# Performance work log

Measured on AMD Instinct MI355X. Metric: run time of the kernel, lower is better.

## Reference

```python
import jax, jax.numpy as jnp
import numpy as np

NUM_EXPERTS = 8
TOP_K = 2

def setup_inputs() -> dict:
    key = jax.random.key(0)
    k1, k2, k3, k4 = jax.random.split(key, 4)
    B, T, C, F = 4, 2048, 1024, 4096
    x = jax.random.normal(k1, (B, T, C), dtype=jnp.float32)
    gate_w = jax.random.normal(k2, (C, NUM_EXPERTS), dtype=jnp.float32) * 0.02
    w1 = jax.random.normal(k3, (NUM_EXPERTS, C, F), dtype=jnp.float32) * 0.02
    w2 = jax.random.normal(k4, (NUM_EXPERTS, F, C), dtype=jnp.float32) * 0.02
    return {"x": x, "gate_w": gate_w, "w1": w1, "w2": w2}

def reference(x, gate_w, w1, w2):
    # Router: softmax over experts, then top-k and renormalize
    router_logits = jnp.einsum('btc,ce->bte', x, gate_w)          # [B,T,E]
    routing = jax.nn.softmax(router_logits, axis=-1)
    topw, topi = jax.lax.top_k(routing, TOP_K)                    # [B,T,K]
    topw = topw / jnp.sum(topw, axis=-1, keepdims=True)
    # Combined per-expert weight per token (zero if not selected)
    onehot = jax.nn.one_hot(topi, NUM_EXPERTS, dtype=x.dtype)     # [B,T,K,E]
    combine = jnp.einsum('btk,btke->bte', topw, onehot)           # [B,T,E]
    # Expert FFNs (exact GELU, matching torch nn.GELU default)
    out = jnp.zeros_like(x)
    for e in range(NUM_EXPERTS):
        h = jax.nn.gelu(jnp.einsum('btc,cf->btf', x, w1[e]), approximate=False)
        y = jnp.einsum('btf,fc->btc', h, w2[e])
        out = out + combine[..., e:e+1] * y
    return out
```

## Files before the change

kernel.cpp:

```cpp
#include <hip/hip_runtime.h>
#include <hip/hip_bf16.h>
#include <math.h>

#define NUM_EXPERTS 8
#define NTOK 8192
#define CDIM 1024
#define FDIM 4096
#define MAXSLOTS 17408
#define MAXTILES 136
#define TILES_PER_XCD 17

typedef __bf16 bf16x8 __attribute__((ext_vector_type(8)));
typedef float  f32x4  __attribute__((ext_vector_type(4)));

#define GPTR(p) ((const __attribute__((address_space(1))) unsigned int*)(p))
#define LPTR(p) ((__attribute__((address_space(3))) unsigned int*)(p))

__device__ __forceinline__ float gelu_exact(float v){
  return 0.5f * v * (1.0f + erff(v * 0.70710678118654752f));
}
__device__ __forceinline__ float bf2f(unsigned short u){
  union { unsigned int i; float f; } cv; cv.i = ((unsigned int)u) << 16; return cv.f;
}

__global__ __launch_bounds__(256) void moe_router(
    const float* __restrict__ x, const float* __restrict__ gw,
    int2* __restrict__ topi, float2* __restrict__ topw, int* __restrict__ counts)
{
  int token = blockIdx.x * 4 + (threadIdx.x >> 6);
  int lane  = threadIdx.x & 63;
  int e = lane & 7, part = lane >> 3;
  const float* xr = x + (size_t)token * CDIM;
  float s = 0.f;
  int c0 = part * 128;
  for (int c = c0; c < c0 + 128; ++c) s += xr[c] * gw[c * 8 + e];
  s += __shfl_xor(s, 8); s += __shfl_xor(s, 16); s += __shfl_xor(s, 32);
  float m1 = s; int i1 = e;
  for (int off = 1; off < 8; off <<= 1){
    float ov = __shfl_xor(m1, off); int oi = __shfl_xor(i1, off);
    if (ov > m1 || (ov == m1 && oi < i1)){ m1 = ov; i1 = oi; }
  }
  float l2 = (e == i1) ? -INFINITY : s;
  float m2 = l2; int i2 = e;
  for (int off = 1; off < 8; off <<= 1){
    float ov = __shfl_xor(m2, off); int oi = __shfl_xor(i2, off);
    if (ov > m2 || (ov == m2 && oi < i2)){ m2 = ov; i2 = oi; }
  }
  if (lane == 0){
    float r = expf(m2 - m1);
    float wa = 1.f / (1.f + r);
    topi[token] = make_int2(i1, i2);
    topw[token] = make_float2(wa, 1.f - wa);
    atomicAdd(&counts[i1], 1);
    atomicAdd(&counts[i2], 1);
  }
}

__global__ __launch_bounds__(256) void convert_x_kernel(
    const float* __restrict__ x, __hip_bfloat16* __restrict__ xb)
{
  int i = (blockIdx.x * 256 + threadIdx.x) * 4;
  float4 v = *(const float4*)(x + i);
  union { __hip_bfloat16 hh[4]; ushort4 u; } cv;
  cv.hh[0] = __float2bfloat16(v.x);
  cv.hh[1] = __float2bfloat16(v.y);
  cv.hh[2] = __float2bfloat16(v.z);
  cv.hh[3] = __float2bfloat16(v.w);
  *(ushort4*)(xb + i) = cv.u;
}

__global__ __launch_bounds__(256) void transpose_bf16_kernel(
    const float* __restrict__ in, __hip_bfloat16* __restrict__ outp, int R, int Cc)
{
  __shared__ __hip_bfloat16 tile[64 * 66];
  const size_t msz = (size_t)R * Cc;
  const float* inm = in + (size_t)blockIdx.z * msz;
  __hip_bfloat16* outm = outp + (size_t)blockIdx.z * msz;
  int r0 = blockIdx.y * 64, c0 = blockIdx.x * 64;
  int t = threadIdx.x;
  int r = t & 63, cseg = (t >> 6) * 16;
  const float* src = inm + (size_t)(r0 + r) * Cc + c0 + cseg;
  float4 v0 = ((const float4*)src)[0];
  float4 v1 = ((const float4*)src)[1];
  float4 v2 = ((const float4*)src)[2];
  float4 v3 = ((const float4*)src)[3];
  float vv[16] = {v0.x,v0.y,v0.z,v0.w, v1.x,v1.y,v1.z,v1.w,
                  v2.x,v2.y,v2.z,v2.w, v3.x,v3.y,v3.z,v3.w};
#pragma unroll
  for (int k = 0; k < 16; ++k)
    tile[(cseg + k) * 66 + r] = __float2bfloat16(vv[k]);
  __syncthreads();
#pragma unroll
  for (int p = 0; p < 2; ++p){
    int cc = p * 32 + (t >> 3), ch = (t & 7) * 8;
    const unsigned short* rowp = (const unsigned short*)tile + cc * 66 + ch;
    unsigned int a = *(const unsigned int*)(rowp + 0);
    unsigned int b = *(const unsigned int*)(rowp + 2);
    unsigned int c = *(const unsigned int*)(rowp + 4);
    unsigned int d = *(const unsigned int*)(rowp + 6);
    *(uint4*)(outm + (size_t)(c0 + cc) * R + r0 + ch) = make_uint4(a, b, c, d);
  }
}

__global__ void scan_kernel(const int* __restrict__ counts, int* cursors, int* num_tiles,
    int* tile_expert, int* tile_slotbase, int* slot_token, float* slot_weight)
{
  int t = threadIdx.x;
  if (t == 0){
    int base = 0, T = 0;
    for (int e = 0; e < NUM_EXPERTS; ++e){
      cursors[e] = base;
      int nt = (counts[e] + 127) >> 7;
      for (int i = 0; i < nt; ++i){ tile_expert[T] = e; tile_slotbase[T] = base + i * 128; ++T; }
      base += nt << 7;
    }
    *num_tiles = T;
  }
  for (int i = t; i < MAXSLOTS; i += 256){ slot_token[i] = 0; slot_weight[i] = 0.f; }
}

__global__ void assign_kernel(const int2* __restrict__ topi, const float2* __restrict__ topw,
    int* cursors, int* slot_token, float* slot_weight, int2* __restrict__ token_slots)
{
  int token = blockIdx.x * 256 + threadIdx.x;
  int2 ii = topi[token];
  float2 ww = topw[token];
  int p0 = atomicAdd(&cursors[ii.x], 1);
  slot_token[p0] = token; slot_weight[p0] = ww.x;
  int p1 = atomicAdd(&cursors[ii.y], 1);
  slot_token[p1] = token; slot_weight[p1] = ww.y;
  token_slots[token] = make_int2(p0, p1);
}

__global__ __launch_bounds__(256) void gemm1_kernel(
    const __hip_bfloat16* __restrict__ xbf, const __hip_bfloat16* __restrict__ w1t,
    __hip_bfloat16* __restrict__ h, const int* __restrict__ num_tiles,
    const int* __restrict__ tile_expert, const int* __restrict__ tile_slotbase,
    const int* __restrict__ slot_token)
{
  __shared__ __align__(16) char smem[32768];
  const int L = blockIdx.x;
  const int xcd = L & 7;
  const int j = L >> 3;
  const int tl = j >> 5;
  const int nb = j & 31;
  const int tm = xcd * TILES_PER_XCD + tl;
  if (tm >= *num_tiles) return;
  const int e = tile_expert[tm];
  const int sbase = tile_slotbase[tm];
  const int n0 = nb * 128;
  const int t = threadIdx.x;
  const int cl = t & 7;
  const __hip_bfloat16* w1e = w1t + (size_t)e * FDIM * CDIM;
  const __hip_bfloat16* aptr[4];
  const __hip_bfloat16* bptr[4];
#pragma unroll
  for (int jj = 0; jj < 4; ++jj){
    int r = jj * 32 + (t >> 3);
    int cg = cl ^ (r & 7);
    int tok = slot_token[sbase + r];
    aptr[jj] = xbf + (size_t)tok * CDIM + cg * 8;
    bptr[jj] = w1e + (size_t)(n0 + r) * CDIM + cg * 8;
  }
  char* asml = smem + t * 16;
  char* bsml = smem + 16384 + t * 16;

  f32x4 acc[4][4] = {};
  const int lane = t & 63, wv = t >> 6;
  const int wm = (wv >> 1) * 64, wn = (wv & 1) * 64;
  const int lrow = lane & 15, quad = lane >> 4;

  for (int k0 = 0; k0 < CDIM; k0 += 64){
    __syncthreads();
#pragma unroll
    for (int jj = 0; jj < 4; ++jj){
      __builtin_amdgcn_global_load_lds(GPTR(aptr[jj] + k0), LPTR(asml + jj * 4096), 16, 0, 0);
      __builtin_amdgcn_global_load_lds(GPTR(bptr[jj] + k0), LPTR(bsml + jj * 4096), 16, 0, 0);
    }
    __syncthreads();
#pragma unroll
    for (int kk = 0; kk < 2; ++kk){
      bf16x8 af[4], bfr[4];
#pragma unroll
      for (int i = 0; i < 4; ++i){
        int ar = wm + i * 16 + lrow;
        int ac = (kk * 4 + quad) ^ (ar & 7);
        af[i] = *(const bf16x8*)(smem + ar * 128 + ac * 16);
        int br = wn + i * 16 + lrow;
        int bc = (kk * 4 + quad) ^ (br & 7);
        bfr[i] = *(const bf16x8*)(smem + 16384 + br * 128 + bc * 16);
      }
#pragma unroll
      for (int i = 0; i < 4; ++i)
#pragma unroll
        for (int jj = 0; jj < 4; ++jj)
          acc[i][jj] = __builtin_amdgcn_mfma_f32_16x16x32_bf16(af[i], bfr[jj], acc[i][jj], 0, 0, 0);
    }
  }
  __syncthreads();
  __hip_bfloat16* Ct = (__hip_bfloat16*)smem;
#pragma unroll
  for (int i = 0; i < 4; ++i)
#pragma unroll
    for (int r = 0; r < 4; ++r){
      int row = wm + i * 16 + quad * 4 + r;
#pragma unroll
      for (int jj = 0; jj < 4; ++jj){
        int col = wn + jj * 16 + lrow;
        int cc = (col >> 3) ^ (row & 15);
        Ct[row * 128 + cc * 8 + (col & 7)] = __float2bfloat16(gelu_exact(acc[i][jj][r]));
      }
    }
  __syncthreads();
#pragma unroll
  for (int v = 0; v < 8; ++v){
    int Lr = v * 256 + t;
    int row = Lr >> 4, cc = Lr & 15;
    int cs = cc ^ (row & 15);
    uint4 val = *(const uint4*)(Ct + row * 128 + cs * 8);
    *(uint4*)(h + (size_t)(sbase + row) * FDIM + n0 + cc * 8) = val;
  }
}

__global__ __launch_bounds__(256) void gemm2_kernel(
    const __hip_bfloat16* __restrict__ h, const __hip_bfloat16* __restrict__ w2t,
    __hip_bfloat16* __restrict__ y, const int* __restrict__ num_tiles,
    const int* __restrict__ tile_expert, const int* __restrict__ tile_slotbase)
{
  __shared__ __align__(16) char smem[32768];
  const int L = blockIdx.x;
  const int xcd = L & 7;
  const int j = L >> 3;
  const int tl = j >> 3;
  const int nb = j & 7;
  const int tm = xcd * TILES_PER_XCD + tl;
  if (tm >= *num_tiles) return;
  const int e = tile_expert[tm];
  const int sbase = tile_slotbase[tm];
  const int n0 = nb * 128;
  const int t = threadIdx.x;
  const int cl = t & 7;
  const __hip_bfloat16* w2e = w2t + (size_t)e * CDIM * FDIM;
  const __hip_bfloat16* aptr[4];
  const __hip_bfloat16* bptr[4];
#pragma unroll
  for (int jj = 0; jj < 4; ++jj){
    int r = jj * 32 + (t >> 3);
    int cg = cl ^ (r & 7);
    aptr[jj] = h   + (size_t)(sbase + r) * FDIM + cg * 8;
    bptr[jj] = w2e + (size_t)(n0 + r)   * FDIM + cg * 8;
  }
  char* asml = smem + t * 16;
  char* bsml = smem + 16384 + t * 16;

  f32x4 acc[4][4] = {};
  const int lane = t & 63, wv = t >> 6;
  const int wm = (wv >> 1) * 64, wn = (wv & 1) * 64;
  const int lrow = lane & 15, quad = lane >> 4;

  for (int k0 = 0; k0 < FDIM; k0 += 64){
    __syncthreads();
#pragma unroll
    for (int jj = 0; jj < 4; ++jj){
      __builtin_amdgcn_global_load_lds(GPTR(aptr[jj] + k0), LPTR(asml + jj * 4096), 16, 0, 0);
      __builtin_amdgcn_global_load_lds(GPTR(bptr[jj] + k0), LPTR(bsml + jj * 4096), 16, 0, 0);
    }
    __syncthreads();
#pragma unroll
    for (int kk = 0; kk < 2; ++kk){
      bf16x8 af[4], bfr[4];
#pragma unroll
      for (int i = 0; i < 4; ++i){
        int ar = wm + i * 16 + lrow;
        int ac = (kk * 4 + quad) ^ (ar & 7);
        af[i] = *(const bf16x8*)(smem + ar * 128 + ac * 16);
        int br = wn + i * 16 + lrow;
        int bc = (kk * 4 + quad) ^ (br & 7);
        bfr[i] = *(const bf16x8*)(smem + 16384 + br * 128 + bc * 16);
      }
#pragma unroll
      for (int i = 0; i < 4; ++i)
#pragma unroll
        for (int jj = 0; jj < 4; ++jj)
          acc[i][jj] = __builtin_amdgcn_mfma_f32_16x16x32_bf16(af[i], bfr[jj], acc[i][jj], 0, 0, 0);
    }
  }
  __syncthreads();
  __hip_bfloat16* Ct = (__hip_bfloat16*)smem;
#pragma unroll
  for (int i = 0; i < 4; ++i)
#pragma unroll
    for (int r = 0; r < 4; ++r){
      int row = wm + i * 16 + quad * 4 + r;
#pragma unroll
      for (int jj = 0; jj < 4; ++jj){
        int col = wn + jj * 16 + lrow;
        int cc = (col >> 3) ^ (row & 15);
        Ct[row * 128 + cc * 8 + (col & 7)] = __float2bfloat16(acc[i][jj][r]);
      }
    }
  __syncthreads();
#pragma unroll
  for (int v = 0; v < 8; ++v){
    int Lr = v * 256 + t;
    int row = Lr >> 4, cc = Lr & 15;
    int cs = cc ^ (row & 15);
    uint4 val = *(const uint4*)(Ct + row * 128 + cs * 8);
    *(uint4*)(y + (size_t)(sbase + row) * CDIM + n0 + cc * 8) = val;
  }
}

__global__ __launch_bounds__(256) void combine_kernel(
    const __hip_bfloat16* __restrict__ y, const int2* __restrict__ token_slots,
    const float* __restrict__ slot_weight, float* __restrict__ out)
{
  int token = blockIdx.x;
  int c = threadIdx.x * 4;
  int2 ss = token_slots[token];
  float w0 = slot_weight[ss.x], w1 = slot_weight[ss.y];
  ushort4 a = *(const ushort4*)((const unsigned short*)y + (size_t)ss.x * CDIM + c);
  ushort4 b = *(const ushort4*)((const unsigned short*)y + (size_t)ss.y * CDIM + c);
  float4 o;
  o.x = w0 * bf2f(a.x) + w1 * bf2f(b.x);
  o.y = w0 * bf2f(a.y) + w1 * bf2f(b.y);
  o.z = w0 * bf2f(a.z) + w1 * bf2f(b.z);
  o.w = w0 * bf2f(a.w) + w1 * bf2f(b.w);
  *(float4*)(out + (size_t)token * CDIM + c) = o;
}

__global__ __launch_bounds__(256) void naive_kernel(
    const float* __restrict__ x, const float* __restrict__ w1, const float* __restrict__ w2,
    const int2* __restrict__ topi, const float2* __restrict__ topw, float* __restrict__ out)
{
  __shared__ float xs[CDIM];
  __shared__ float hs[FDIM];
  int token = blockIdx.x;
  int t = threadIdx.x;
  for (int i = t; i < CDIM; i += 256) xs[i] = x[(size_t)token * CDIM + i];
  float acc[4] = {0.f, 0.f, 0.f, 0.f};
  int2 ei = topi[token]; float2 ew = topw[token];
  int elist[2] = {ei.x, ei.y}; float wlist[2] = {ew.x, ew.y};
  for (int kk = 0; kk < 2; ++kk){
    int e = elist[kk]; float wgt = wlist[kk];
    __syncthreads();
    for (int f = t; f < FDIM; f += 256){
      const float* wcol = w1 + (size_t)e * CDIM * FDIM + f;
      float s = 0.f;
      for (int c = 0; c < CDIM; ++c) s += xs[c] * wcol[(size_t)c * FDIM];
      hs[f] = gelu_exact(s);
    }
    __syncthreads();
    for (int ii = 0; ii < 4; ++ii){
      int c = ii * 256 + t;
      const float* w2col = w2 + (size_t)e * FDIM * CDIM + c;
      float s = 0.f;
      for (int f = 0; f < FDIM; ++f) s += hs[f] * w2col[(size_t)f * CDIM];
      acc[ii] += wgt * s;
    }
  }
  for (int ii = 0; ii < 4; ++ii) out[(size_t)token * CDIM + ii * 256 + t] = acc[ii];
}

extern "C" void kernel_launch(void* const* d_in, const int* in_sizes, int n_in,
                              void* d_out, int out_size, void* d_ws, size_t ws_size,
                              hipStream_t stream)
{
  const float* x  = (const float*)d_in[0];
  const float* gw = (const float*)d_in[1];
  const float* w1 = (const float*)d_in[2];
  const float* w2 = (const float*)d_in[3];
  float* out = (float*)d_out;
  char* ws = (char*)d_ws;

  int*    counts        = (int*)(ws + 0);
  int*    cursors       = (int*)(ws + 32);
  int*    num_tiles     = (int*)(ws + 64);
  int*    tile_expert   = (int*)(ws + 256);
  int*    tile_slotbase = (int*)(ws + 1024);
  int2*   topi          = (int2*)(ws + 4096);
  float2* topw          = (float2*)(ws + 69632);
  int*    slot_token    = (int*)(ws + 135168);
  float*  slot_weight   = (float*)(ws + 204800);
  int2*   token_slots   = (int2*)(ws + 278528);
  const size_t XBF_OFF = 1u << 20;
  const size_t W1T_OFF = XBF_OFF + (size_t)NTOK * CDIM * 2;
  const size_t W2T_OFF = W1T_OFF + (size_t)NUM_EXPERTS * CDIM * FDIM * 2;
  const size_t H_OFF   = W2T_OFF + (size_t)NUM_EXPERTS * CDIM * FDIM * 2;
  const size_t NEED    = H_OFF + (size_t)MAXSLOTS * FDIM * 2;
  __hip_bfloat16* xbf = (__hip_bfloat16*)(ws + XBF_OFF);
  __hip_bfloat16* w1t = (__hip_bfloat16*)(ws + W1T_OFF);
  __hip_bfloat16* w2t = (__hip_bfloat16*)(ws + W2T_OFF);
  __hip_bfloat16* h   = (__hip_bfloat16*)(ws + H_OFF);
  __hip_bfloat16* y   = (__hip_bfloat16*)(ws + W1T_OFF);

  hipMemsetAsync(ws, 0, 4096, stream);

  moe_router<<<NTOK / 4, 256, 0, stream>>>(x, gw, topi, topw, counts);

  if (ws_size >= NEED){
    convert_x_kernel<<<NTOK * CDIM / (4 * 256), 256, 0, stream>>>(x, xbf);
    transpose_bf16_kernel<<<dim3(FDIM / 64, CDIM / 64, NUM_EXPERTS), 256, 0, stream>>>(w1, w1t, CDIM, FDIM);
    transpose_bf16_kernel<<<dim3(CDIM / 64, FDIM / 64, NUM_EXPERTS), 256, 0, stream>>>(w2, w2t, FDIM, CDIM);
    scan_kernel<<<1, 256, 0, stream>>>(counts, cursors, num_tiles, tile_expert, tile_slotbase, slot_token, slot_weight);
    assign_kernel<<<NTOK / 256, 256, 0, stream>>>(topi, topw, cursors, slot_token, slot_weight, token_slots);
    gemm1_kernel<<<8 * TILES_PER_XCD * 32, 256, 0, stream>>>(xbf, w1t, h, num_tiles, tile_expert, tile_slotbase, slot_token);
    gemm2_kernel<<<8 * TILES_PER_XCD * 8, 256, 0, stream>>>(h, w2t, y, num_tiles, tile_expert, tile_slotbase);
    combine_kernel<<<NTOK, 256, 0, stream>>>(y, token_slots, slot_weight, out);
  } else {
    naive_kernel<<<NTOK, 256, 0, stream>>>(x, w1, w2, topi, topw, out);
  }
}
```

Before: 1.137 ms.

## Unify expert GEMMs into templated 128x256-tile kernel with triple-buffered LDS pipeline

Replaces the two separate expert GEMM kernels with one templated kernel. It uses 512 threads, a 128x256 output tile, and a three-stage LDS ring of 32-wide K slices filled by global_load_lds, so the next slices are prefetched while MFMAs run. Plain __syncthreads is replaced by vmcnt waits plus barriers and s_setprio around the MFMA groups, and the epilogue writes bf16 results straight from registers instead of staging them through LDS. This trades a larger LDS footprint (72KB per block) and more live registers for more data reuse per tile and overlap of loads with compute. The LDS layout has no swizzle, so bank conflicts are possible.

```diff
diff --git a/kernel.cpp b/kernel.cpp
--- a/kernel.cpp
+++ b/kernel.cpp
@@ -132,181 +132,124 @@
   token_slots[token] = make_int2(p0, p1);
 }
 
-__global__ __launch_bounds__(256) void gemm1_kernel(
-    const __hip_bfloat16* __restrict__ xbf, const __hip_bfloat16* __restrict__ w1t,
-    __hip_bfloat16* __restrict__ h, const int* __restrict__ num_tiles,
-    const int* __restrict__ tile_expert, const int* __restrict__ tile_slotbase,
-    const int* __restrict__ slot_token)
-{
-  __shared__ __align__(16) char smem[32768];
+template<int KD, int ND, bool G1>
+__global__ __launch_bounds__(512, 4) void moe_gemm(
+    const __hip_bfloat16* __restrict__ A, const __hip_bfloat16* __restrict__ Bw,
+    __hip_bfloat16* __restrict__ Out,
+    const int* __restrict__ num_tiles, const int* __restrict__ tile_expert,
+    const int* __restrict__ tile_slotbase, const int* __restrict__ slot_token)
+{
+  constexpr int NT = KD / 32;
+  constexpr int NBLK = ND / 256;
+  __shared__ __align__(16) char smem[73728];
   const int L = blockIdx.x;
   const int xcd = L & 7;
-  const int j = L >> 3;
-  const int tl = j >> 5;
-  const int nb = j & 31;
+  const int jdec = L >> 3;
+  const int tl = jdec / NBLK;
+  const int nb = jdec % NBLK;
   const int tm = xcd * TILES_PER_XCD + tl;
   if (tm >= *num_tiles) return;
   const int e = tile_expert[tm];
   const int sbase = tile_slotbase[tm];
-  const int n0 = nb * 128;
+  const int n0 = nb * 256;
   const int t = threadIdx.x;
-  const int cl = t & 7;
-  const __hip_bfloat16* w1e = w1t + (size_t)e * FDIM * CDIM;
-  const __hip_bfloat16* aptr[4];
-  const __hip_bfloat16* bptr[4];
+  const int lane = t & 63, wid = t >> 6;
+  const int wm = wid >> 2, wn = wid & 3;
+  const int lr = lane & 15, lq = lane >> 4;
+
+  const int arowi = sbase + wid * 16 + lr;
+  const int arow = G1 ? slot_token[arowi] : arowi;
+  const __hip_bfloat16* srcA  = A  + (size_t)arow * KD + lq * 8;
+  const __hip_bfloat16* srcB0 = Bw + ((size_t)e * ND + n0 + wid * 16 + lr) * KD + lq * 8;
+  const __hip_bfloat16* srcB1 = srcB0 + (size_t)128 * KD;
+  char* dA  = smem + wid * 1024;
+  char* dB0 = smem + 24576 + wid * 1024;
+  char* dB1 = dB0 + 8192;
+
+#define STG_A(kt, ss) __builtin_amdgcn_global_load_lds(GPTR(srcA + (size_t)(kt) * 32), LPTR(dA + (ss) * 8192), 16, 0, 0)
+#define STG_B(kt, ss) do{ \
+    __builtin_amdgcn_global_load_lds(GPTR(srcB0 + (size_t)(kt) * 32), LPTR(dB0 + (ss) * 16384), 16, 0, 0); \
+    __builtin_amdgcn_global_load_lds(GPTR(srcB1 + (size_t)(kt) * 32), LPTR(dB1 + (ss) * 16384), 16, 0, 0); }while(0)
+
+  STG_A(0, 0); STG_B(0, 0);
+  STG_A(1, 1); STG_B(1, 1);
+
+  f32x4 acc[4][4] = {};
+  const char* rdA = smem + (wm * 4) * 1024 + lane * 16;
+  const char* rdB = smem + 24576 + (wn * 4) * 1024 + lane * 16;
+
+  asm volatile("s_waitcnt vmcnt(3)\n\ts_barrier" ::: "memory");
+  __builtin_amdgcn_sched_barrier(0);
+
+  int s = 0;
+  for (int kt = 0; kt < NT; ++kt){
+    int s2 = s + 2; if (s2 >= 3) s2 -= 3;
+    const char* pA = rdA + s * 8192;
+    const char* pB = rdB + s * 16384;
+    bf16x8 b0 = *(const bf16x8*)(pB);
+    bf16x8 b1 = *(const bf16x8*)(pB + 1024);
+    bf16x8 b2 = *(const bf16x8*)(pB + 2048);
+    bf16x8 b3 = *(const bf16x8*)(pB + 3072);
+    bf16x8 a0 = *(const bf16x8*)(pA);
+    bf16x8 a1 = *(const bf16x8*)(pA + 1024);
+    if (kt + 2 < NT) STG_A(kt + 2, s2);
+    __builtin_amdgcn_s_setprio(1);
+    acc[0][0] = __builtin_amdgcn_mfma_f32_16x16x32_bf16(b0, a0, acc[0][0], 0, 0, 0);
+    acc[0][1] = __builtin_amdgcn_mfma_f32_16x16x32_bf16(b1, a0, acc[0][1], 0, 0, 0);
+    acc[0][2] = __builtin_amdgcn_mfma_f32_16x16x32_bf16(b2, a0, acc[0][2], 0, 0, 0);
+    acc[0][3] = __builtin_amdgcn_mfma_f32_16x16x32_bf16(b3, a0, acc[0][3], 0, 0, 0);
+    acc[1][0] = __builtin_amdgcn_mfma_f32_16x16x32_bf16(b0, a1, acc[1][0], 0, 0, 0);
+    acc[1][1] = __builtin_amdgcn_mfma_f32_16x16x32_bf16(b1, a1, acc[1][1], 0, 0, 0);
+    acc[1][2] = __builtin_amdgcn_mfma_f32_16x16x32_bf16(b2, a1, acc[1][2], 0, 0, 0);
+    acc[1][3] = __builtin_amdgcn_mfma_f32_16x16x32_bf16(b3, a1, acc[1][3], 0, 0, 0);
+    __builtin_amdgcn_s_setprio(0);
+    a0 = *(const bf16x8*)(pA + 2048);
+    a1 = *(const bf16x8*)(pA + 3072);
+    if (kt + 2 < NT) STG_B(kt + 2, s2);
+    __builtin_amdgcn_s_setprio(1);
+    acc[2][0] = __builtin_amdgcn_mfma_f32_16x16x32_bf16(b0, a0, acc[2][0], 0, 0, 0);
+    acc[2][1] = __builtin_amdgcn_mfma_f32_16x16x32_bf16(b1, a0, acc[2][1], 0, 0, 0);
+    acc[2][2] = __builtin_amdgcn_mfma_f32_16x16x32_bf16(b2, a0, acc[2][2], 0, 0, 0);
+    acc[2][3] = __builtin_amdgcn_mfma_f32_16x16x32_bf16(b3, a0, acc[2][3], 0, 0, 0);
+    acc[3][0] = __builtin_amdgcn_mfma_f32_16x16x32_bf16(b0, a1, acc[3][0], 0, 0, 0);
+    acc[3][1] = __builtin_amdgcn_mfma_f32_16x16x32_bf16(b1, a1, acc[3][1], 0, 0, 0);
+    acc[3][2] = __builtin_amdgcn_mfma_f32_16x16x32_bf16(b2, a1, acc[3][2], 0, 0, 0);
+    acc[3][3] = __builtin_amdgcn_mfma_f32_16x16x32_bf16(b3, a1, acc[3][3], 0, 0, 0);
+    __builtin_amdgcn_s_setprio(0);
+    if (kt < NT - 2){
+      asm volatile("s_waitcnt vmcnt(3)\n\ts_barrier" ::: "memory");
+      __builtin_amdgcn_sched_barrier(0);
+    } else if (kt < NT - 1){
+      asm volatile("s_waitcnt vmcnt(0)\n\ts_barrier" ::: "memory");
+      __builtin_amdgcn_sched_barrier(0);
+    }
+    s = (s == 2) ? 0 : s + 1;
+  }
+#undef STG_A
+#undef STG_B
+
+  const int orow0 = sbase + wm * 64 + lr;
+  const int ocol0 = n0 + wn * 64 + lq * 4;
 #pragma unroll
-  for (int jj = 0; jj < 4; ++jj){
-    int r = jj * 32 + (t >> 3);
-    int cg = cl ^ (r & 7);
-    int tok = slot_token[sbase + r];
-    aptr[jj] = xbf + (size_t)tok * CDIM + cg * 8;
-    bptr[jj] = w1e + (size_t)(n0 + r) * CDIM + cg * 8;
-  }
-  char* asml = smem + t * 16;
-  char* bsml = smem + 16384 + t * 16;
-
-  f32x4 acc[4][4] = {};
-  const int lane = t & 63, wv = t >> 6;
-  const int wm = (wv >> 1) * 64, wn = (wv & 1) * 64;
-  const int lrow = lane & 15, quad = lane >> 4;
-
-  for (int k0 = 0; k0 < CDIM; k0 += 64){
-    __syncthreads();
+  for (int i = 0; i < 4; ++i){
+    __hip_bfloat16* orow = Out + (size_t)(orow0 + i * 16) * ND + ocol0;
 #pragma unroll
-    for (int jj = 0; jj < 4; ++jj){
-      __builtin_amdgcn_global_load_lds(GPTR(aptr[jj] + k0), LPTR(asml + jj * 4096), 16, 0, 0);
-      __builtin_amdgcn_global_load_lds(GPTR(bptr[jj] + k0), LPTR(bsml + jj * 4096), 16, 0, 0);
-    }
-    __syncthreads();
-#pragma unroll
-    for (int kk = 0; kk < 2; ++kk){
-      bf16x8 af[4], bfr[4];
-#pragma unroll
-      for (int i = 0; i < 4; ++i){
-        int ar = wm + i * 16 + lrow;
-        int ac = (kk * 4 + quad) ^ (ar & 7);
-        af[i] = *(const bf16x8*)(smem + ar * 128 + ac * 16);
-        int br = wn + i * 16 + lrow;
-        int bc = (kk * 4 + quad) ^ (br & 7);
-        bfr[i] = *(const bf16x8*)(smem + 16384 + br * 128 + bc * 16);
+    for (int j2 = 0; j2 < 4; ++j2){
+      f32x4 v = acc[i][j2];
+      union { __hip_bfloat16 h4[4]; ushort4 u; } cv;
+      if (G1){
+        cv.h4[0] = __float2bfloat16(gelu_exact(v[0]));
+        cv.h4[1] = __float2bfloat16(gelu_exact(v[1]));
+        cv.h4[2] = __float2bfloat16(gelu_exact(v[2]));
+        cv.h4[3] = __float2bfloat16(gelu_exact(v[3]));
+      } else {
+        cv.h4[0] = __float2bfloat16(v[0]);
+        cv.h4[1] = __float2bfloat16(v[1]);
+        cv.h4[2] = __float2bfloat16(v[2]);
+        cv.h4[3] = __float2bfloat16(v[3]);
       }
-#pragma unroll
-      for (int i = 0; i < 4; ++i)
-#pragma unroll
-        for (int jj = 0; jj < 4; ++jj)
-          acc[i][jj] = __builtin_amdgcn_mfma_f32_16x16x32_bf16(af[i], bfr[jj], acc[i][jj], 0, 0, 0);
-    }
-  }
-  __syncthreads();
-  __hip_bfloat16* Ct = (__hip_bfloat16*)smem;
-#pragma unroll
-  for (int i = 0; i < 4; ++i)
-#pragma unroll
-    for (int r = 0; r < 4; ++r){
-      int row = wm + i * 16 + quad * 4 + r;
-#pragma unroll
-      for (int jj = 0; jj < 4; ++jj){
-        int col = wn + jj * 16 + lrow;
-        int cc = (col >> 3) ^ (row & 15);
-        Ct[row * 128 + cc * 8 + (col & 7)] = __float2bfloat16(gelu_exact(acc[i][jj][r]));
-      }
-    }
-  __syncthreads();
-#pragma unroll
-  for (int v = 0; v < 8; ++v){
-    int Lr = v * 256 + t;
-    int row = Lr >> 4, cc = Lr & 15;
-    int cs = cc ^ (row & 15);
-    uint4 val = *(const uint4*)(Ct + row * 128 + cs * 8);
-    *(uint4*)(h + (size_t)(sbase + row) * FDIM + n0 + cc * 8) = val;
-  }
-}
-
-__global__ __launch_bounds__(256) void gemm2_kernel(
-    const __hip_bfloat16* __restrict__ h, const __hip_bfloat16* __restrict__ w2t,
-    __hip_bfloat16* __restrict__ y, const int* __restrict__ num_tiles,
-    const int* __restrict__ tile_expert, const int* __restrict__ tile_slotbase)
-{
-  __shared__ __align__(16) char smem[32768];
-  const int L = blockIdx.x;
-  const int xcd = L & 7;
-  const int j = L >> 3;
-  const int tl = j >> 3;
-  const int nb = j & 7;
-  const int tm = xcd * TILES_PER_XCD + tl;
-  if (tm >= *num_tiles) return;
-  const int e = tile_expert[tm];
-  const int sbase = tile_slotbase[tm];
-  const int n0 = nb * 128;
-  const int t = threadIdx.x;
-  const int cl = t & 7;
-  const __hip_bfloat16* w2e = w2t + (size_t)e * CDIM * FDIM;
-  const __hip_bfloat16* aptr[4];
-  const __hip_bfloat16* bptr[4];
-#pragma unroll
-  for (int jj = 0; jj < 4; ++jj){
-    int r = jj * 32 + (t >> 3);
-    int cg = cl ^ (r & 7);
-    aptr[jj] = h   + (size_t)(sbase + r) * FDIM + cg * 8;
-    bptr[jj] = w2e + (size_t)(n0 + r)   * FDIM + cg * 8;
-  }
-  char* asml = smem + t * 16;
-  char* bsml = smem + 16384 + t * 16;
-
-  f32x4 acc[4][4] = {};
-  const int lane = t & 63, wv = t >> 6;
-  const int wm = (wv >> 1) * 64, wn = (wv & 1) * 64;
-  const int lrow = lane & 15, quad = lane >> 4;
-
-  for (int k0 = 0; k0 < FDIM; k0 += 64){
-    __syncthreads();
-#pragma unroll
-    for (int jj = 0; jj < 4; ++jj){
-      __builtin_amdgcn_global_load_lds(GPTR(aptr[jj] + k0), LPTR(asml + jj * 4096), 16, 0, 0);
-      __builtin_amdgcn_global_load_lds(GPTR(bptr[jj] + k0), LPTR(bsml + jj * 4096), 16, 0, 0);
-    }
-    __syncthreads();
-#pragma unroll
-    for (int kk = 0; kk < 2; ++kk){
-      bf16x8 af[4], bfr[4];
-#pragma unroll
-      for (int i = 0; i < 4; ++i){
-        int ar = wm + i * 16 + lrow;
-        int ac = (kk * 4 + quad) ^ (ar & 7);
-        af[i] = *(const bf16x8*)(smem + ar * 128 + ac * 16);
-        int br = wn + i * 16 + lrow;
-        int bc = (kk * 4 + quad) ^ (br & 7);
-        bfr[i] = *(const bf16x8*)(smem + 16384 + br * 128 + bc * 16);
-      }
-#pragma unroll
-      for (int i = 0; i < 4; ++i)
-#pragma unroll
-        for (int jj = 0; jj < 4; ++jj)
-          acc[i][jj] = __builtin_amdgcn_mfma_f32_16x16x32_bf16(af[i], bfr[jj], acc[i][jj], 0, 0, 0);
-    }
-  }
-  __syncthreads();
-  __hip_bfloat16* Ct = (__hip_bfloat16*)smem;
-#pragma unroll
-  for (int i = 0; i < 4; ++i)
-#pragma unroll
-    for (int r = 0; r < 4; ++r){
-      int row = wm + i * 16 + quad * 4 + r;
-#pragma unroll
-      for (int jj = 0; jj < 4; ++jj){
-        int col = wn + jj * 16 + lrow;
-        int cc = (col >> 3) ^ (row & 15);
-        Ct[row * 128 + cc * 8 + (col & 7)] = __float2bfloat16(acc[i][jj][r]);
-      }
-    }
-  __syncthreads();
-#pragma unroll
-  for (int v = 0; v < 8; ++v){
-    int Lr = v * 256 + t;
-    int row = Lr >> 4, cc = Lr & 15;
-    int cs = cc ^ (row & 15);
-    uint4 val = *(const uint4*)(Ct + row * 128 + cs * 8);
-    *(uint4*)(y + (size_t)(sbase + row) * CDIM + n0 + cc * 8) = val;
+      *(ushort4*)(orow + j2 * 16) = cv.u;
+    }
   }
 }
 
@@ -403,8 +346,10 @@
     transpose_bf16_kernel<<<dim3(CDIM / 64, FDIM / 64, NUM_EXPERTS), 256, 0, stream>>>(w2, w2t, FDIM, CDIM);
     scan_kernel<<<1, 256, 0, stream>>>(counts, cursors, num_tiles, tile_expert, tile_slotbase, slot_token, slot_weight);
     assign_kernel<<<NTOK / 256, 256, 0, stream>>>(topi, topw, cursors, slot_token, slot_weight, token_slots);
-    gemm1_kernel<<<8 * TILES_PER_XCD * 32, 256, 0, stream>>>(xbf, w1t, h, num_tiles, tile_expert, tile_slotbase, slot_token);
-    gemm2_kernel<<<8 * TILES_PER_XCD * 8, 256, 0, stream>>>(h, w2t, y, num_tiles, tile_expert, tile_slotbase);
+    moe_gemm<CDIM, FDIM, true ><<<8 * TILES_PER_XCD * (FDIM / 256), 512, 0, stream>>>(
+        xbf, w1t, h, num_tiles, tile_expert, tile_slotbase, slot_token);
+    moe_gemm<FDIM, CDIM, false><<<8 * TILES_PER_XCD * (CDIM / 256), 512, 0, stream>>>(
+        h, w2t, y, num_tiles, tile_expert, tile_slotbase, slot_token);
     combine_kernel<<<NTOK, 256, 0, stream>>>(y, token_slots, slot_weight, out);
   } else {
     naive_kernel<<<NTOK, 256, 0, stream>>>(x, w1, w2, topi, topw, out);
```

Result: no change. 1.132 ms (-0.4%).
